# Kernel tuning notes

Hardware: AMD Instinct MI355X
Metric: run time of the kernel (lower is better)

## Reference

```python
import jax, jax.numpy as jnp
import numpy as np

H, S, B, R, IN, NN, OP = 512, 256, 32, 16, 4, 16, 6
NEG = -1.0e12


def setup_inputs() -> dict:
    key = jax.random.key(0)
    ks = jax.random.split(key, 40)
    f32 = jnp.float32
    inp = {}
    inp["node_emb"] = jax.random.normal(ks[0], (B, 1, H), f32)
    inp["left"] = jax.random.normal(ks[1], (B, 1, H), f32)
    inp["encoder_outputs"] = jax.random.normal(ks[2], (S, B, H), f32)
    inp["num_pades"] = jax.random.normal(ks[3], (B, NN, H), f32)
    inp["formula_scores"] = jax.random.normal(ks[4], (R, H), f32)
    inp["has_left"] = jax.random.bernoulli(ks[5], 0.5, (B,))
    lengths = jax.random.randint(ks[6], (B,), S // 2, S + 1)
    inp["seq_mask"] = jnp.arange(S)[None, :] >= lengths[:, None]
    nlen = jax.random.randint(ks[7], (B,), (IN + NN) // 2, IN + NN + 1)
    inp["mask_nums"] = jnp.arange(IN + NN)[None, :] >= nlen[:, None]
    sc = 0.04  # init scale for weights
    def w(i, shape):
        return jax.random.normal(ks[i], shape, f32) * sc
    inp["embedding_weight"] = jax.random.normal(ks[8], (1, IN, H), f32)
    inp["Wcl"] = w(9, (H, H));    inp["bcl"] = jnp.zeros((H,), f32)
    inp["Wclg"] = w(10, (H, H));  inp["bclg"] = jnp.zeros((H,), f32)
    inp["Wcr"] = w(11, (2 * H, H));  inp["bcr"] = jnp.zeros((H,), f32)
    inp["Wcrg"] = w(12, (2 * H, H)); inp["bcrg"] = jnp.zeros((H,), f32)
    inp["Wops"] = w(13, (2 * H, OP)); inp["bops"] = jnp.zeros((OP,), f32)
    inp["Wattn"] = w(14, (2 * H, H)); inp["battn"] = jnp.zeros((H,), f32)
    inp["wattn_s"] = w(15, (H,));     inp["battn_s"] = jnp.zeros((), f32)
    inp["Wfattn"] = w(16, (2 * H, H)); inp["bfattn"] = jnp.zeros((H,), f32)
    inp["wfattn_s"] = w(17, (H,));     inp["bfattn_s"] = jnp.zeros((), f32)
    inp["Wscore"] = w(18, (3 * H, H)); inp["bscore"] = jnp.zeros((H,), f32)
    inp["wscore_s"] = w(19, (H,))  # Score.score has no bias
    inp["Wfp1"] = w(20, (H, H));   inp["bfp1"] = jnp.zeros((H,), f32)
    inp["Wfp2"] = w(21, (H,));     inp["bfp2"] = jnp.zeros((), f32)
    return inp


def _forward(node_emb, left, has_left, encoder_outputs, num_pades, seq_mask,
             mask_nums, formula_scores, embedding_weight, Wcl, bcl, Wclg, bclg,
             Wcr, bcr, Wcrg, bcrg, Wops, bops, Wattn, battn, wattn_s, battn_s,
             Wfattn, bfattn, wfattn_s, bfattn_s, Wscore, bscore, wscore_s,
             Wfp1, bfp1, Wfp2, bfp2):
    # gated left/right node update (dropout = identity, eval mode)
    c = node_emb                                            # [B,1,H]
    lc = jnp.concatenate([left, c], axis=-1)                # [B,1,2H]
    out_l = jnp.tanh(c @ Wcl + bcl) * jax.nn.sigmoid(c @ Wclg + bclg)
    out_r = jnp.tanh(lc @ Wcr + bcr) * jax.nn.sigmoid(lc @ Wcrg + bcrg)
    current_node = jnp.where(has_left[:, None, None], out_r, out_l)  # [B,1,H]
    # TreeAttn(current_node, encoder_outputs): additive attention over S
    Wh, We = Wattn[:H], Wattn[H:]
    feat = jnp.tanh(current_node[:, 0][None] @ Wh + encoder_outputs @ We + battn)  # [S,B,H]
    en = (feat @ wattn_s + battn_s).T                       # [B,S]
    en = jnp.where(seq_mask, NEG, en)
    current_attn = jax.nn.softmax(en, axis=1)[:, None, :]   # [B,1,S]
    eo_b = jnp.transpose(encoder_outputs, (1, 0, 2))        # [B,S,H]
    current_context = current_attn @ eo_b                   # [B,1,H]
    # embedding table = learned constants + numbers from the problem
    emb_w = jnp.concatenate(
        [jnp.broadcast_to(embedding_weight, (node_emb.shape[0], IN, H)), num_pades], axis=1)  # [B,IN+NN,H]
    leaf_input = jnp.concatenate([current_node, current_context], axis=2)[:, 0]  # [B,2H]
    # FormulaAttn: additive attention of each formula over all tokens
    Wfe, Wff = Wfattn[:H], Wfattn[H:]
    ffeat = jnp.tanh(encoder_outputs[None] @ Wfe
                     + (formula_scores @ Wff)[:, None, None, :] + bfattn)  # [R,S,B,H]
    fen = jnp.transpose(ffeat @ wfattn_s + bfattn_s, (2, 0, 1))            # [B,R,S]
    fen = jnp.where(seq_mask[:, None, :], NEG, fen)
    formulas_attn = jax.nn.softmax(fen, axis=-1)            # [B,R,S]
    formulas_context = (formulas_attn + 0.2 * current_attn) @ eo_b         # [B,R,H]
    formula_feat = jnp.tanh(formulas_context @ Wfp1 + bfp1)
    formula_prob = jax.nn.softmax(formula_feat @ Wfp2 + bfp2, axis=-1)     # [B,R]
    # Score over candidate number embeddings
    N = IN + NN
    hid = jnp.broadcast_to(leaf_input[:, None, :], (leaf_input.shape[0], N, 2 * H))
    ein = jnp.concatenate([hid, emb_w], axis=-1)            # [B,N,3H]
    ns = jnp.tanh(ein @ Wscore + bscore) @ wscore_s         # [B,N]
    num_score = jnp.where(mask_nums, NEG, ns)
    op = leaf_input @ Wops + bops                           # [B,OP]
    return (num_score, op, current_node, current_context, emb_w, formula_prob)


def reference(node_emb, left, has_left, encoder_outputs, num_pades, seq_mask,
              mask_nums, formula_scores, embedding_weight, Wcl, bcl, Wclg, bclg,
              Wcr, bcr, Wcrg, bcrg, Wops, bops, Wattn, battn, wattn_s, battn_s,
              Wfattn, bfattn, wfattn_s, bfattn_s, Wscore, bscore, wscore_s,
              Wfp1, bfp1, Wfp2, bfp2):
    return _forward(node_emb, left, has_left, encoder_outputs, num_pades,
                    seq_mask, mask_nums, formula_scores, embedding_weight,
                    Wcl, bcl, Wclg, bclg, Wcr, bcr, Wcrg, bcrg, Wops, bops,
                    Wattn, battn, wattn_s, battn_s, Wfattn, bfattn, wfattn_s,
                    bfattn_s, Wscore, bscore, wscore_s, Wfp1, bfp1, Wfp2, bfp2)
```

## Files before the change

### kernel.cpp

```cpp
#include <hip/hip_runtime.h>
#include <hip/hip_bf16.h>
#include <stdint.h>

#define H 512
#define S 256
#define B 32
#define R 16
#define NEG -1000000000000.0f

typedef unsigned short u16;
typedef short short8 __attribute__((ext_vector_type(8)));
typedef float f32x4 __attribute__((ext_vector_type(4)));

__device__ __forceinline__ float bf2f(u16 u) {
  unsigned int v = ((unsigned int)u) << 16;
  float f; __builtin_memcpy(&f, &v, 4); return f;
}
__device__ __forceinline__ u16 f2u(float x) {
  __hip_bfloat16 h = __float2bfloat16(x);
  u16 u; __builtin_memcpy(&u, &h, 2); return u;
}
__device__ __forceinline__ float ftanh(float x) {
  float e = __expf(2.f * x);
  return 1.f - 2.f * __builtin_amdgcn_rcpf(e + 1.f);
}
__device__ __forceinline__ float ptanh(float x) {
  float xc = fminf(4.f, fmaxf(-4.f, x));
  float x2 = xc * xc;
  float num = xc * (945.f + x2 * (105.f + x2));
  float den = 945.f + x2 * (420.f + 15.f * x2);
  return num * __builtin_amdgcn_rcpf(den);
}
__device__ __forceinline__ float fsig(float x) {
  return __builtin_amdgcn_rcpf(1.f + __expf(-x));
}
__device__ __forceinline__ void gload16(const void* g, void* l) {
  __builtin_amdgcn_global_load_lds(
      (const __attribute__((address_space(1))) unsigned int*)g,
      (__attribute__((address_space(3))) unsigned int*)l, 16, 0, 0);
}

__device__ __forceinline__ void trans_tile(const float* __restrict__ src, int nb, int k0,
                                           u16* __restrict__ dst, int n0, int Krows,
                                           float (*tile)[65], int t) {
  #pragma unroll
  for (int it = 0; it < 16; ++it) {
    int f = it * 256 + t; int r = f >> 6, c = f & 63;
    tile[r][c] = src[(size_t)(k0 + r) * 512 + nb + c];
  }
  __syncthreads();
  #pragma unroll
  for (int it = 0; it < 16; ++it) {
    int f = it * 256 + t; int r = f >> 6, c = f & 63;
    dst[(size_t)(n0 + r) * Krows + k0 + c] = f2u(tile[c][r]);
  }
}

__global__ __launch_bounds__(256) void k_prep1(
    const float* __restrict__ enc, u16* __restrict__ encb, u16* __restrict__ encc,
    const float* __restrict__ Wattn, const float* __restrict__ Wfattn, u16* __restrict__ Wt,
    const float* __restrict__ Wscore, u16* __restrict__ Wt2a, u16* __restrict__ Wt2b,
    const float* __restrict__ Wfp1, u16* __restrict__ Wt3,
    u16* __restrict__ Wt4,
    const float* __restrict__ node_emb, const float* __restrict__ left,
    const int* __restrict__ has_left,
    const float* __restrict__ Wcl, const float* __restrict__ Wclg,
    const float* __restrict__ Wcr, const float* __restrict__ Wcrg,
    float* __restrict__ gp1, float* __restrict__ gp2,
    const float* __restrict__ emb_w, const float* __restrict__ num_pades,
    float* __restrict__ out_embw, u16* __restrict__ embb, u16* __restrict__ leafb) {
  __shared__ float tile[64][65];
  __shared__ float x[128];
  int id = blockIdx.x, t = threadIdx.x;
  if (id < 2048) {
    int i = (id * 256 + t) * 8;
    float4 a = *(const float4*)(enc + i);
    float4 b4 = *(const float4*)(enc + i + 4);
    short8 o;
    o[0] = (short)f2u(a.x); o[1] = (short)f2u(a.y); o[2] = (short)f2u(a.z); o[3] = (short)f2u(a.w);
    o[4] = (short)f2u(b4.x); o[5] = (short)f2u(b4.y); o[6] = (short)f2u(b4.z); o[7] = (short)f2u(b4.w);
    *(short8*)(encb + i) = o;
    int s = i >> 14, b = (i >> 9) & 31, h = i & 511;
    *(short8*)(encc + (((size_t)b << 8) + s) * 512 + h) = o;
  } else if (id < 2176) {
    int f = id - 2048; int gx = f & 15, gy = f >> 4;
    int n0 = gx * 64, k0 = gy * 64;
    const float* src = (n0 < 512) ? (Wattn + 512 * 512) : Wfattn;
    int nb = (n0 < 512) ? n0 : n0 - 512;
    trans_tile(src, nb, k0, Wt, n0, 512, tile, t);
  } else if (id < 2240) {
    int f = id - 2176; int gx = f & 7, gy = f >> 3;
    trans_tile(Wscore + 1024 * 512, gx * 64, gy * 64, Wt2a, gx * 64, 512, tile, t);
  } else if (id < 2368) {
    int f = id - 2240; int gx = f & 7, gy = f >> 3;
    trans_tile(Wscore, gx * 64, gy * 64, Wt2b, gx * 64, 1024, tile, t);
  } else if (id < 2432) {
    int f = id - 2368; int gx = f & 7, gy = f >> 3;
    trans_tile(Wfp1, gx * 64, gy * 64, Wt3, gx * 64, 512, tile, t);
  } else if (id < 2560) {
    int f = id - 2432; int gx = f & 15, gy = f >> 4;
    int n0 = gx * 64, k0 = gy * 64;
    const float* src = (n0 < 512) ? Wattn : (Wfattn + 512 * 512);
    int nb = (n0 < 512) ? n0 : n0 - 512;
    trans_tile(src, nb, k0, Wt4, n0, 512, tile, t);
  } else if (id < 2816) {
    int f = id - 2560;
    int b = f >> 3, kc = f & 7;
    int hl = has_left[b];
    int k0 = kc * 128;
    float* o1 = gp1 + ((size_t)b * 8 + kc) * 512;
    float* o2 = gp2 + ((size_t)b * 8 + kc) * 512;
    if (!hl && kc >= 4) { o1[t] = 0.f; o1[t + 256] = 0.f; o2[t] = 0.f; o2[t + 256] = 0.f; return; }
    if (t < 128) {
      int k = k0 + t;
      x[t] = hl ? (k < 512 ? left[b * 512 + k] : node_emb[b * 512 + k - 512])
                : node_emb[b * 512 + k];
    }
    __syncthreads();
    const float* W1 = hl ? Wcr : Wcl;
    const float* W2 = hl ? Wcrg : Wclg;
    float a1 = 0.f, a2 = 0.f, a3 = 0.f, a4 = 0.f;
    for (int kk = 0; kk < 128; ++kk) {
      float xv = x[kk];
      const float* w1r = W1 + (size_t)(k0 + kk) * 512;
      const float* w2r = W2 + (size_t)(k0 + kk) * 512;
      a1 += xv * w1r[t]; a2 += xv * w1r[t + 256];
      a3 += xv * w2r[t]; a4 += xv * w2r[t + 256];
    }
    o1[t] = a1; o1[t + 256] = a2; o2[t] = a3; o2[t + 256] = a4;
  } else if (id < 3136) {
    int f = id - 2816;
    #pragma unroll
    for (int rr = 0; rr < 2; ++rr) {
      int row = f * 2 + rr;
      int n = row % 20, b = row / 20;
      #pragma unroll
      for (int i = 0; i < 2; ++i) {
        int h = t + 256 * i;
        float v = (n < 4) ? emb_w[n * 512 + h] : num_pades[((size_t)b * 16 + n - 4) * 512 + h];
        out_embw[(size_t)row * 512 + h] = v;
        embb[(size_t)row * 512 + h] = f2u(v);
      }
    }
  } else {
    int f = id - 3136;
    int base = 32 * 1024 + (f * 256 + t) * 16;
    short8 z8 = {0,0,0,0,0,0,0,0};
    *(short8*)(leafb + base) = z8;
    *(short8*)(leafb + base + 8) = z8;
  }
}

template <int FM, int FN>
__device__ __forceinline__ void gemm_body(
    const u16* __restrict__ A, const u16* __restrict__ Bt,
    u16* __restrict__ C16, float* __restrict__ C32,
    int lda, int ldb, int ldc, int ksteps,
    int bm, int bn, int kbase, long zoff,
    u16* As, u16* Bs) {
  constexpr int BM = FM * 32, BN = FN * 32;
  const int tid = threadIdx.x;
  const int lane = tid & 63;
  const int wid = tid >> 6;
  const int wr = (wid >> 1) * (FM * 16);
  const int wc = (wid & 1) * (FN * 16);
  f32x4 acc[FM][FN];
  #pragma unroll
  for (int m = 0; m < FM; ++m)
    #pragma unroll
    for (int n = 0; n < FN; ++n)
      #pragma unroll
      for (int q = 0; q < 4; ++q) acc[m][n][q] = 0.f;

  const int kb = (lane >> 4) * 8;
  const int rr = lane & 15;
  for (int ks = 0; ks < ksteps; ++ks) {
    int k0 = kbase + ks * 32;
    #pragma unroll
    for (int it = 0; it < BM / 64; ++it) {
      int c = it * 256 + tid;
      gload16(A + (size_t)(bm + (c >> 2)) * lda + k0 + (c & 3) * 8, As + c * 8);
    }
    #pragma unroll
    for (int it = 0; it < BN / 64; ++it) {
      int c = it * 256 + tid;
      gload16(Bt + (size_t)(bn + (c >> 2)) * ldb + k0 + (c & 3) * 8, Bs + c * 8);
    }
    __syncthreads();
    short8 af[FM], bf[FN];
    #pragma unroll
    for (int m = 0; m < FM; ++m)
      af[m] = *(const short8*)(As + (wr + m * 16 + rr) * 32 + kb);
    #pragma unroll
    for (int n = 0; n < FN; ++n)
      bf[n] = *(const short8*)(Bs + (wc + n * 16 + rr) * 32 + kb);
    #pragma unroll
    for (int m = 0; m < FM; ++m)
      #pragma unroll
      for (int n = 0; n < FN; ++n)
        acc[m][n] = __builtin_amdgcn_mfma_f32_16x16x32_bf16(af[m], bf[n], acc[m][n], 0, 0, 0);
    __syncthreads();
  }
  int r0 = (lane >> 4) * 4, cc = lane & 15;
  #pragma unroll
  for (int m = 0; m < FM; ++m)
    #pragma unroll
    for (int n = 0; n < FN; ++n)
      #pragma unroll
      for (int q = 0; q < 4; ++q) {
        long row = bm + wr + m * 16 + r0 + q;
        long col = bn + wc + n * 16 + cc;
        if (C16) C16[zoff + row * ldc + col] = f2u(acc[m][n][q]);
        else     C32[zoff + row * ldc + col] = acc[m][n][q];
      }
}

__global__ __launch_bounds__(256) void k_g1(
    const u16* __restrict__ encb, const u16* __restrict__ Wt, u16* __restrict__ EW,
    const u16* __restrict__ cnfs, const u16* __restrict__ Wt4, float* __restrict__ CWFW,
    const u16* __restrict__ embb, const u16* __restrict__ Wt2a, float* __restrict__ Tep) {
  __shared__ u16 As[128 * 32];
  __shared__ u16 Bs[128 * 32];
  int q = blockIdx.x;
  if (q < 512) {
    int x = q & 63, y = q >> 6;
    gemm_body<4, 4>(encb, Wt, EW, nullptr, 512, 512, 1024, 16, x * 128, y * 128, 0, 0, As, Bs);
  } else if (q < 520) {
    int y = q - 512;
    gemm_body<4, 4>(cnfs, Wt4, nullptr, CWFW, 512, 512, 1024, 16, 0, y * 128, 0, 0, As, Bs);
  } else {
    int q2 = q - 520;
    int x = q2 % 10, y = (q2 / 10) % 8, z = q2 / 80;
    gemm_body<2, 2>(embb, Wt2a, nullptr, Tep, 512, 512, 512, 8,
                    x * 64, y * 64, z * 8 * 32, (long)z * 327680, As, Bs);
  }
}

__global__ __launch_bounds__(256) void k_tt(
    const u16* __restrict__ leafb, const u16* __restrict__ Wt2b, float* __restrict__ Tlp,
    const u16* __restrict__ fctxb, const u16* __restrict__ Wt3, float* __restrict__ T3p,
    const float* __restrict__ leaf, const float* __restrict__ Wops,
    const float* __restrict__ bops, float* __restrict__ out_op) {
  __shared__ u16 As[64 * 32];
  __shared__ u16 Bs[64 * 32];
  __shared__ float red[4];
  int q = blockIdx.x;
  if (q < 32) {
    int y = q % 8, z = q / 8;
    gemm_body<2, 2>(leafb, Wt2b, nullptr, Tlp, 1024, 1024, 512, 8,
                    0, y * 64, z * 8 * 32, (long)z * 32768, As, Bs);
  } else if (q < 288) {
    int q2 = q - 32;
    int x = q2 % 8, y = (q2 / 8) % 8, z = q2 / 64;
    gemm_body<2, 2>(fctxb, Wt3, nullptr, T3p, 512, 512, 512, 4,
                    x * 64, y * 64, z * 4 * 32, (long)z * 262144, As, Bs);
  } else {
    int f = q - 288; int o = f % 6, b = f / 6;
    int t = threadIdx.x, w = t >> 6, lane = t & 63;
    float acc = 0.f;
    #pragma unroll
    for (int i = 0; i < 4; ++i) {
      int k = t + 256 * i;
      acc += leaf[b * 1024 + k] * Wops[(size_t)k * 6 + o];
    }
    for (int off = 32; off >= 1; off >>= 1) acc += __shfl_down(acc, off);
    if (lane == 0) red[w] = acc;
    __syncthreads();
    if (t == 0) out_op[b * 6 + o] = red[0] + red[1] + red[2] + red[3] + bops[o];
  }
}

__global__ __launch_bounds__(256) void k_p2(
    const float* __restrict__ gp1, const float* __restrict__ gp2,
    const int* __restrict__ has_left,
    const float* __restrict__ bcl, const float* __restrict__ bclg,
    const float* __restrict__ bcr, const float* __restrict__ bcrg,
    const float* __restrict__ fs,
    float* __restrict__ cur_node, float* __restrict__ out_cn, u16* __restrict__ cnfs) {
  int id = blockIdx.x, t = threadIdx.x;
  if (id < 32) {
    int b = id, hl = has_left[b];
    #pragma unroll
    for (int i = 0; i < 2; ++i) {
      int h = t + 256 * i;
      float s1 = 0.f, s2 = 0.f;
      #pragma unroll
      for (int c = 0; c < 8; ++c) {
        s1 += gp1[((size_t)b * 8 + c) * 512 + h];
        s2 += gp2[((size_t)b * 8 + c) * 512 + h];
      }
      float v = ftanh(s1 + (hl ? bcr[h] : bcl[h])) * fsig(s2 + (hl ? bcrg[h] : bclg[h]));
      cur_node[b * 512 + h] = v;
      out_cn[b * 512 + h] = v;
      cnfs[b * 512 + h] = f2u(v);
    }
  } else if (id < 48) {
    int r = id - 32;
    #pragma unroll
    for (int i = 0; i < 2; ++i) {
      int h = t + 256 * i;
      cnfs[id * 512 + h] = f2u(fs[r * 512 + h]);
    }
  } else {
    #pragma unroll
    for (int i = 0; i < 2; ++i) cnfs[id * 512 + t + 256 * i] = 0;
  }
}

__global__ __launch_bounds__(256) void k_enfen(
    const u16* __restrict__ EW, const float* __restrict__ CWFW,
    const float* __restrict__ battn, const float* __restrict__ bfattn,
    const float* __restrict__ wattn_s, const float* __restrict__ battn_s,
    const float* __restrict__ wfattn_s, const float* __restrict__ bfattn_s,
    const int* __restrict__ seq_mask, float* __restrict__ en, float* __restrict__ fen) {
  __shared__ float sFW[16 * 512];
  __shared__ float swf[512], swa[512], scw[512];
  int bid = blockIdx.x;
  int b = bid >> 5;
  int s0 = (bid & 31) * 8;
  int t = threadIdx.x;
  #pragma unroll
  for (int q = 0; q < 32; ++q) {
    int flat = q * 256 + t;
    int r = flat >> 9, h = flat & 511;
    sFW[flat] = CWFW[(size_t)(32 + r) * 1024 + 512 + h] + bfattn[h];
  }
  swf[t] = wfattn_s[t]; swf[256 + t] = wfattn_s[256 + t];
  swa[t] = wattn_s[t];  swa[256 + t] = wattn_s[256 + t];
  scw[t] = CWFW[(size_t)b * 1024 + t] + battn[t];
  scw[256 + t] = CWFW[(size_t)b * 1024 + 256 + t] + battn[256 + t];
  __syncthreads();
  int w = t >> 6, lane = t & 63;
  int sA = s0 + w * 2, sB = sA + 1;
  int mA = seq_mask[b * 256 + sA], mB = seq_mask[b * 256 + sB];
  if (mA && mB) {
    if (lane == 0) {
      en[b * 256 + sA] = NEG; en[b * 256 + sB] = NEG;
      for (int r = 0; r < 16; ++r) {
        fen[((size_t)b * 16 + r) * 256 + sA] = NEG;
        fen[((size_t)b * 16 + r) * 256 + sB] = NEG;
      }
    }
    return;
  }
  const u16* ewA = EW + (size_t)(sA * 32 + b) * 1024;
  const u16* ewB = EW + (size_t)(sB * 32 + b) * 1024;
  float ewfA[8], ewfB[8], wfv[8];
  float accA = 0.f, accB = 0.f;
  #pragma unroll
  for (int i = 0; i < 8; ++i) {
    int h = lane + 64 * i;
    float cw = scw[h], wa = swa[h];
    accA += ptanh(cw + bf2f(ewA[h])) * wa;
    accB += ptanh(cw + bf2f(ewB[h])) * wa;
    ewfA[i] = bf2f(ewA[512 + h]);
    ewfB[i] = bf2f(ewB[512 + h]);
    wfv[i] = swf[h];
  }
  for (int o = 32; o >= 1; o >>= 1) {
    accA += __shfl_down(accA, o);
    accB += __shfl_down(accB, o);
  }
  if (lane == 0) {
    en[b * 256 + sA] = mA ? NEG : (accA + battn_s[0]);
    en[b * 256 + sB] = mB ? NEG : (accB + battn_s[0]);
  }
  for (int r = 0; r < 16; ++r) {
    float a0 = 0.f, a1 = 0.f;
    #pragma unroll
    for (int i = 0; i < 8; ++i) {
      int h = lane + 64 * i;
      float fwv = sFW[r * 512 + h];
      a0 += ptanh(fwv + ewfA[i]) * wfv[i];
      a1 += ptanh(fwv + ewfB[i]) * wfv[i];
    }
    for (int o = 32; o >= 1; o >>= 1) {
      a0 += __shfl_down(a0, o);
      a1 += __shfl_down(a1, o);
    }
    if (lane == 0) {
      fen[((size_t)b * 16 + r) * 256 + sA] = mA ? NEG : (a0 + bfattn_s[0]);
      fen[((size_t)b * 16 + r) * 256 + sB] = mB ? NEG : (a1 + bfattn_s[0]);
    }
  }
}

__global__ __launch_bounds__(512) void k_ctxall(
    const float* __restrict__ en, const float* __restrict__ fen,
    const u16* __restrict__ encc, const float* __restrict__ cur_node,
    float* __restrict__ out_ctx, float* __restrict__ leaf, u16* __restrict__ fctxb,
    u16* __restrict__ leafb) {
  int br = blockIdx.x;
  int b = br / 9, k = br % 9;
  int t = threadIdx.x;
  __shared__ float red[512];
  __shared__ float sa0[256], sa1[256];
  float xe = (t < 256) ? en[b * 256 + t] : NEG;
  red[t] = xe; __syncthreads();
  for (int o = 256; o > 0; o >>= 1) { if (t < o) red[t] = fmaxf(red[t], red[t + o]); __syncthreads(); }
  float m = red[0]; __syncthreads();
  float ee = (t < 256) ? __expf(xe - m) : 0.f;
  red[t] = ee; __syncthreads();
  for (int o = 256; o > 0; o >>= 1) { if (t < o) red[t] += red[t + o]; __syncthreads(); }
  float attn_v = ee / red[0];
  __syncthreads();
  const u16* eb = encc + (size_t)b * 131072;
  if (k < 8) {
    #pragma unroll
    for (int p = 0; p < 2; ++p) {
      int j = k + p * 8;
      float xf = (t < 256) ? fen[((size_t)b * 16 + j) * 256 + t] : NEG;
      red[t] = xf; __syncthreads();
      for (int o = 256; o > 0; o >>= 1) { if (t < o) red[t] = fmaxf(red[t], red[t + o]); __syncthreads(); }
      float mf = red[0]; __syncthreads();
      float ef = (t < 256) ? __expf(xf - mf) : 0.f;
      red[t] = ef; __syncthreads();
      for (int o = 256; o > 0; o >>= 1) { if (t < o) red[t] += red[t + o]; __syncthreads(); }
      float coef = ef / red[0] + 0.2f * attn_v;
      __syncthreads();
      if (t < 256) { if (p == 0) sa0[t] = coef; else sa1[t] = coef; }
    }
    __syncthreads();
    int h = t;
    float acc0 = 0.f, acc1 = 0.f;
    #pragma unroll 8
    for (int s = 0; s < 256; ++s) {
      float ev = bf2f(eb[(size_t)s * 512 + h]);
      acc0 += sa0[s] * ev;
      acc1 += sa1[s] * ev;
    }
    fctxb[((size_t)b * 16 + k) * 512 + h] = f2u(acc0);
    fctxb[((size_t)b * 16 + k + 8) * 512 + h] = f2u(acc1);
  } else {
    if (t < 256) sa0[t] = attn_v;
    __syncthreads();
    int h = t;
    float acc = 0.f;
    #pragma unroll 8
    for (int s = 0; s < 256; ++s)
      acc += sa0[s] * bf2f(eb[(size_t)s * 512 + h]);
    float cn = cur_node[b * 512 + h];
    out_ctx[b * 512 + h] = acc;
    leaf[b * 1024 + 512 + h] = acc;
    leaf[b * 1024 + h] = cn;
    leafb[b * 1024 + h] = f2u(cn);
    leafb[b * 1024 + 512 + h] = f2u(acc);
  }
}

__global__ __launch_bounds__(256) void k_epi(
    const float* __restrict__ Tep, const float* __restrict__ Tlp,
    const float* __restrict__ bscore,
    const float* __restrict__ wscore_s, const int* __restrict__ mask_nums,
    float* __restrict__ out_ns,
    const float* __restrict__ T3p, const float* __restrict__ bfp1,
    const float* __restrict__ Wfp2, const float* __restrict__ bfp2,
    float* __restrict__ out_fp) {
  int id = blockIdx.x, t = threadIdx.x;
  int w = t >> 6, lane = t & 63;
  __shared__ float red[16];
  if (id < 640) {
    int row = id;
    int b = row / 20;
    float acc = 0.f;
    #pragma unroll
    for (int i = 0; i < 2; ++i) {
      int h = t + 256 * i;
      float tv = bscore[h];
      #pragma unroll
      for (int z = 0; z < 2; ++z) tv += Tep[(size_t)z * 327680 + (size_t)row * 512 + h];
      #pragma unroll
      for (int z = 0; z < 4; ++z) tv += Tlp[(size_t)z * 32768 + (size_t)b * 512 + h];
      acc += ftanh(tv) * wscore_s[h];
    }
    for (int o = 32; o >= 1; o >>= 1) acc += __shfl_down(acc, o);
    if (lane == 0) red[w] = acc;
    __syncthreads();
    if (t == 0) out_ns[row] = mask_nums[row] ? NEG : (red[0] + red[1] + red[2] + red[3]);
  } else {
    int b = id - 640;
    #pragma unroll
    for (int j2 = 0; j2 < 4; ++j2) {
      int j = w * 4 + j2;
      int row = b * 16 + j;
      float acc = 0.f;
      #pragma unroll
      for (int i = 0; i < 8; ++i) {
        int h = lane + 64 * i;
        float v = bfp1[h];
        #pragma unroll
        for (int z = 0; z < 4; ++z) v += T3p[(size_t)z * 262144 + (size_t)row * 512 + h];
        acc += ftanh(v) * Wfp2[h];
      }
      for (int o = 32; o >= 1; o >>= 1) acc += __shfl_down(acc, o);
      if (lane == 0) red[j] = acc + bfp2[0];
    }
    __syncthreads();
    if (t < 16) {
      float xx = red[t];
      float mm = xx;
      for (int o = 8; o >= 1; o >>= 1) mm = fmaxf(mm, __shfl_xor(mm, o, 16));
      float e = __expf(xx - mm);
      float s2 = e;
      for (int o = 8; o >= 1; o >>= 1) s2 += __shfl_xor(s2, o, 16);
      out_fp[b * 16 + t] = e / s2;
    }
  }
}

extern "C" void kernel_launch(void* const* d_in, const int* in_sizes, int n_in,
                              void* d_out, int out_size, void* d_ws, size_t ws_size,
                              hipStream_t stream) {
  const float* node_emb  = (const float*)d_in[0];
  const float* left      = (const float*)d_in[1];
  const float* enc       = (const float*)d_in[2];
  const float* num_pades = (const float*)d_in[3];
  const float* fs        = (const float*)d_in[4];
  const int*   has_left  = (const int*)d_in[5];
  const int*   seq_mask  = (const int*)d_in[6];
  const int*   mask_nums = (const int*)d_in[7];
  const float* emb_w     = (const float*)d_in[8];
  const float* Wcl  = (const float*)d_in[9];
  const float* bcl  = (const float*)d_in[10];
  const float* Wclg = (const float*)d_in[11];
  const float* bclg = (const float*)d_in[12];
  const float* Wcr  = (const float*)d_in[13];
  const float* bcr  = (const float*)d_in[14];
  const float* Wcrg = (const float*)d_in[15];
  const float* bcrg = (const float*)d_in[16];
  const float* Wops = (const float*)d_in[17];
  const float* bops = (const float*)d_in[18];
  const float* Wattn   = (const float*)d_in[19];
  const float* battn   = (const float*)d_in[20];
  const float* wattn_s = (const float*)d_in[21];
  const float* battn_s = (const float*)d_in[22];
  const float* Wfattn   = (const float*)d_in[23];
  const float* bfattn   = (const float*)d_in[24];
  const float* wfattn_s = (const float*)d_in[25];
  const float* bfattn_s = (const float*)d_in[26];
  const float* Wscore   = (const float*)d_in[27];
  const float* bscore   = (const float*)d_in[28];
  const float* wscore_s = (const float*)d_in[29];
  const float* Wfp1 = (const float*)d_in[30];
  const float* bfp1 = (const float*)d_in[31];
  const float* Wfp2 = (const float*)d_in[32];
  const float* bfp2 = (const float*)d_in[33];

  float* out = (float*)d_out;
  float* out_ns   = out + 0;
  float* out_op   = out + 640;
  float* out_cn   = out + 832;
  float* out_ctx  = out + 17216;
  float* out_embw = out + 33600;
  float* out_fp   = out + 361280;

  uint8_t* wsb = (uint8_t*)d_ws;
  u16*   encb = (u16*)(wsb + 0);
  u16*   Wt   = (u16*)(wsb + 8388608);
  u16*   Wt2a = (u16*)(wsb + 9437184);
  u16*   Wt2b = (u16*)(wsb + 9961472);
  u16*   Wt3  = (u16*)(wsb + 11010048);
  u16*   Wt4  = (u16*)(wsb + 11534336);
  u16*   EW   = (u16*)(wsb + 12582912);
  u16*   embb = (u16*)(wsb + 29360128);
  u16*   leafb= (u16*)(wsb + 30015488);
  u16*   cnfs = (u16*)(wsb + 30146560);
  float* CWFW = (float*)(wsb + 30277632);
  float* Tep  = (float*)(wsb + 30801920);
  float* Tlp  = (float*)(wsb + 36044800);
  float* T3p  = (float*)(wsb + 36569088);
  float* fb   = (float*)(wsb + 40763392);
  float* cur_node = fb + 0;
  float* en   = fb + 16384;
  float* fen  = fb + 24576;
  float* leaf = fb + 155648;
  u16*   fctxb= (u16*)(fb + 188416);
  float* gp1  = fb + 319488;
  float* gp2  = fb + 450560;
  u16*   encc = (u16*)(wsb + 45088768);

  k_prep1<<<3144, 256, 0, stream>>>(enc, encb, encc, Wattn, Wfattn, Wt, Wscore, Wt2a, Wt2b,
                                    Wfp1, Wt3, Wt4,
                                    node_emb, left, has_left, Wcl, Wclg, Wcr, Wcrg,
                                    gp1, gp2, emb_w, num_pades, out_embw, embb, leafb);
  k_p2<<<128, 256, 0, stream>>>(gp1, gp2, has_left, bcl, bclg, bcr, bcrg, fs,
                                cur_node, out_cn, cnfs);
  k_g1<<<680, 256, 0, stream>>>(encb, Wt, EW, cnfs, Wt4, CWFW, embb, Wt2a, Tep);
  k_enfen<<<1024, 256, 0, stream>>>(EW, CWFW, battn, bfattn, wattn_s, battn_s,
                                    wfattn_s, bfattn_s, seq_mask, en, fen);
  k_ctxall<<<288, 512, 0, stream>>>(en, fen, encc, cur_node, out_ctx, leaf, fctxb, leafb);
  k_tt<<<480, 256, 0, stream>>>(leafb, Wt2b, Tlp, fctxb, Wt3, T3p,
                                leaf, Wops, bops, out_op);
  k_epi<<<672, 256, 0, stream>>>(Tep, Tlp, bscore, wscore_s, mask_nums, out_ns,
                                 T3p, bfp1, Wfp2, bfp2, out_fp);
}
```

Measured before the change: 99.27 us.

## Coarsen enfen, ctxall and tt kernels to amortize shared setup per block

k_enfen now handles four sequence positions per wavefront instead of two, which halves the blocks that reload the 32KB sFW table from CWFW. k_ctxall computes four formula contexts per block instead of two, so each encoder column read is reused across more accumulators and the repeated softmax over en runs in fewer blocks. The k_tt GEMMs use larger split-K chunks, which halves the partial buffers that k_epi has to sum. In exchange there are fewer blocks, so parallelism and occupancy drop, and the wider kernels use more registers.

```diff
diff --git a/kernel.cpp b/kernel.cpp
--- a/kernel.cpp
+++ b/kernel.cpp
@@ -245,17 +245,17 @@
   __shared__ u16 Bs[64 * 32];
   __shared__ float red[4];
   int q = blockIdx.x;
-  if (q < 32) {
+  if (q < 16) {
     int y = q % 8, z = q / 8;
-    gemm_body<2, 2>(leafb, Wt2b, nullptr, Tlp, 1024, 1024, 512, 8,
-                    0, y * 64, z * 8 * 32, (long)z * 32768, As, Bs);
-  } else if (q < 288) {
-    int q2 = q - 32;
+    gemm_body<2, 2>(leafb, Wt2b, nullptr, Tlp, 1024, 1024, 512, 16,
+                    0, y * 64, z * 16 * 32, (long)z * 32768, As, Bs);
+  } else if (q < 144) {
+    int q2 = q - 16;
     int x = q2 % 8, y = (q2 / 8) % 8, z = q2 / 64;
-    gemm_body<2, 2>(fctxb, Wt3, nullptr, T3p, 512, 512, 512, 4,
-                    x * 64, y * 64, z * 4 * 32, (long)z * 262144, As, Bs);
+    gemm_body<2, 2>(fctxb, Wt3, nullptr, T3p, 512, 512, 512, 8,
+                    x * 64, y * 64, z * 8 * 32, (long)z * 262144, As, Bs);
   } else {
-    int f = q - 288; int o = f % 6, b = f / 6;
+    int f = q - 144; int o = f % 6, b = f / 6;
     int t = threadIdx.x, w = t >> 6, lane = t & 63;
     float acc = 0.f;
     #pragma unroll
@@ -316,8 +316,8 @@
   __shared__ float sFW[16 * 512];
   __shared__ float swf[512], swa[512], scw[512];
   int bid = blockIdx.x;
-  int b = bid >> 5;
-  int s0 = (bid & 31) * 8;
+  int b = bid >> 4;
+  int s0 = (bid & 15) * 16;
   int t = threadIdx.x;
   #pragma unroll
   for (int q = 0; q < 32; ++q) {
@@ -331,56 +331,65 @@
   scw[256 + t] = CWFW[(size_t)b * 1024 + 256 + t] + battn[256 + t];
   __syncthreads();
   int w = t >> 6, lane = t & 63;
-  int sA = s0 + w * 2, sB = sA + 1;
-  int mA = seq_mask[b * 256 + sA], mB = seq_mask[b * 256 + sB];
-  if (mA && mB) {
+  int sbase = s0 + w * 4;
+  int msk[4];
+  int allm = 1;
+  #pragma unroll
+  for (int p = 0; p < 4; ++p) { msk[p] = seq_mask[b * 256 + sbase + p]; allm &= msk[p]; }
+  if (allm) {
     if (lane == 0) {
-      en[b * 256 + sA] = NEG; en[b * 256 + sB] = NEG;
-      for (int r = 0; r < 16; ++r) {
-        fen[((size_t)b * 16 + r) * 256 + sA] = NEG;
-        fen[((size_t)b * 16 + r) * 256 + sB] = NEG;
-      }
+      #pragma unroll
+      for (int p = 0; p < 4; ++p) en[b * 256 + sbase + p] = NEG;
+      for (int r = 0; r < 16; ++r)
+        #pragma unroll
+        for (int p = 0; p < 4; ++p)
+          fen[((size_t)b * 16 + r) * 256 + sbase + p] = NEG;
     }
     return;
   }
-  const u16* ewA = EW + (size_t)(sA * 32 + b) * 1024;
-  const u16* ewB = EW + (size_t)(sB * 32 + b) * 1024;
-  float ewfA[8], ewfB[8], wfv[8];
-  float accA = 0.f, accB = 0.f;
+  const u16* ew[4];
+  #pragma unroll
+  for (int p = 0; p < 4; ++p) ew[p] = EW + (size_t)((sbase + p) * 32 + b) * 1024;
+  float ewf[4][8], wfv[8];
+  float accE[4] = {0.f, 0.f, 0.f, 0.f};
   #pragma unroll
   for (int i = 0; i < 8; ++i) {
     int h = lane + 64 * i;
     float cw = scw[h], wa = swa[h];
-    accA += ptanh(cw + bf2f(ewA[h])) * wa;
-    accB += ptanh(cw + bf2f(ewB[h])) * wa;
-    ewfA[i] = bf2f(ewA[512 + h]);
-    ewfB[i] = bf2f(ewB[512 + h]);
+    #pragma unroll
+    for (int p = 0; p < 4; ++p) {
+      accE[p] += ptanh(cw + bf2f(ew[p][h])) * wa;
+      ewf[p][i] = bf2f(ew[p][512 + h]);
+    }
     wfv[i] = swf[h];
   }
   for (int o = 32; o >= 1; o >>= 1) {
-    accA += __shfl_down(accA, o);
-    accB += __shfl_down(accB, o);
+    #pragma unroll
+    for (int p = 0; p < 4; ++p) accE[p] += __shfl_down(accE[p], o);
   }
   if (lane == 0) {
-    en[b * 256 + sA] = mA ? NEG : (accA + battn_s[0]);
-    en[b * 256 + sB] = mB ? NEG : (accB + battn_s[0]);
+    #pragma unroll
+    for (int p = 0; p < 4; ++p)
+      en[b * 256 + sbase + p] = msk[p] ? NEG : (accE[p] + battn_s[0]);
   }
   for (int r = 0; r < 16; ++r) {
-    float a0 = 0.f, a1 = 0.f;
+    float a[4] = {0.f, 0.f, 0.f, 0.f};
     #pragma unroll
     for (int i = 0; i < 8; ++i) {
       int h = lane + 64 * i;
       float fwv = sFW[r * 512 + h];
-      a0 += ptanh(fwv + ewfA[i]) * wfv[i];
-      a1 += ptanh(fwv + ewfB[i]) * wfv[i];
+      float wf = wfv[i];
+      #pragma unroll
+      for (int p = 0; p < 4; ++p) a[p] += ptanh(fwv + ewf[p][i]) * wf;
     }
     for (int o = 32; o >= 1; o >>= 1) {
-      a0 += __shfl_down(a0, o);
-      a1 += __shfl_down(a1, o);
+      #pragma unroll
+      for (int p = 0; p < 4; ++p) a[p] += __shfl_down(a[p], o);
     }
     if (lane == 0) {
-      fen[((size_t)b * 16 + r) * 256 + sA] = mA ? NEG : (a0 + bfattn_s[0]);
-      fen[((size_t)b * 16 + r) * 256 + sB] = mB ? NEG : (a1 + bfattn_s[0]);
+      #pragma unroll
+      for (int p = 0; p < 4; ++p)
+        fen[((size_t)b * 16 + r) * 256 + sbase + p] = msk[p] ? NEG : (a[p] + bfattn_s[0]);
     }
   }
 }
@@ -391,10 +400,10 @@
     float* __restrict__ out_ctx, float* __restrict__ leaf, u16* __restrict__ fctxb,
     u16* __restrict__ leafb) {
   int br = blockIdx.x;
-  int b = br / 9, k = br % 9;
+  int b = br / 5, k = br % 5;
   int t = threadIdx.x;
   __shared__ float red[512];
-  __shared__ float sa0[256], sa1[256];
+  __shared__ float sa[4][256];
   float xe = (t < 256) ? en[b * 256 + t] : NEG;
   red[t] = xe; __syncthreads();
   for (int o = 256; o > 0; o >>= 1) { if (t < o) red[t] = fmaxf(red[t], red[t + o]); __syncthreads(); }
@@ -405,10 +414,10 @@
   float attn_v = ee / red[0];
   __syncthreads();
   const u16* eb = encc + (size_t)b * 131072;
-  if (k < 8) {
-    #pragma unroll
-    for (int p = 0; p < 2; ++p) {
-      int j = k + p * 8;
+  if (k < 4) {
+    #pragma unroll
+    for (int p = 0; p < 4; ++p) {
+      int j = k + p * 4;
       float xf = (t < 256) ? fen[((size_t)b * 16 + j) * 256 + t] : NEG;
       red[t] = xf; __syncthreads();
       for (int o = 256; o > 0; o >>= 1) { if (t < o) red[t] = fmaxf(red[t], red[t + o]); __syncthreads(); }
@@ -418,27 +427,31 @@
       for (int o = 256; o > 0; o >>= 1) { if (t < o) red[t] += red[t + o]; __syncthreads(); }
       float coef = ef / red[0] + 0.2f * attn_v;
       __syncthreads();
-      if (t < 256) { if (p == 0) sa0[t] = coef; else sa1[t] = coef; }
+      if (t < 256) sa[p][t] = coef;
     }
     __syncthreads();
     int h = t;
-    float acc0 = 0.f, acc1 = 0.f;
-    #pragma unroll 8
+    float acc0 = 0.f, acc1 = 0.f, acc2 = 0.f, acc3 = 0.f;
+    #pragma unroll 4
     for (int s = 0; s < 256; ++s) {
       float ev = bf2f(eb[(size_t)s * 512 + h]);
-      acc0 += sa0[s] * ev;
-      acc1 += sa1[s] * ev;
+      acc0 += sa[0][s] * ev;
+      acc1 += sa[1][s] * ev;
+      acc2 += sa[2][s] * ev;
+      acc3 += sa[3][s] * ev;
     }
     fctxb[((size_t)b * 16 + k) * 512 + h] = f2u(acc0);
-    fctxb[((size_t)b * 16 + k + 8) * 512 + h] = f2u(acc1);
+    fctxb[((size_t)b * 16 + k + 4) * 512 + h] = f2u(acc1);
+    fctxb[((size_t)b * 16 + k + 8) * 512 + h] = f2u(acc2);
+    fctxb[((size_t)b * 16 + k + 12) * 512 + h] = f2u(acc3);
   } else {
-    if (t < 256) sa0[t] = attn_v;
+    if (t < 256) sa[0][t] = attn_v;
     __syncthreads();
     int h = t;
     float acc = 0.f;
     #pragma unroll 8
     for (int s = 0; s < 256; ++s)
-      acc += sa0[s] * bf2f(eb[(size_t)s * 512 + h]);
+      acc += sa[0][s] * bf2f(eb[(size_t)s * 512 + h]);
     float cn = cur_node[b * 512 + h];
     out_ctx[b * 512 + h] = acc;
     leaf[b * 1024 + 512 + h] = acc;
@@ -470,7 +483,7 @@
       #pragma unroll
       for (int z = 0; z < 2; ++z) tv += Tep[(size_t)z * 327680 + (size_t)row * 512 + h];
       #pragma unroll
-      for (int z = 0; z < 4; ++z) tv += Tlp[(size_t)z * 32768 + (size_t)b * 512 + h];
+      for (int z = 0; z < 2; ++z) tv += Tlp[(size_t)z * 32768 + (size_t)b * 512 + h];
       acc += ftanh(tv) * wscore_s[h];
     }
     for (int o = 32; o >= 1; o >>= 1) acc += __shfl_down(acc, o);
@@ -489,7 +502,7 @@
         int h = lane + 64 * i;
         float v = bfp1[h];
         #pragma unroll
-        for (int z = 0; z < 4; ++z) v += T3p[(size_t)z * 262144 + (size_t)row * 512 + h];
+        for (int z = 0; z < 2; ++z) v += T3p[(size_t)z * 262144 + (size_t)row * 512 + h];
         acc += ftanh(v) * Wfp2[h];
       }
       for (int o = 32; o >= 1; o >>= 1) acc += __shfl_down(acc, o);
@@ -586,10 +599,10 @@
   k_p2<<<128, 256, 0, stream>>>(gp1, gp2, has_left, bcl, bclg, bcr, bcrg, fs,
                                 cur_node, out_cn, cnfs);
   k_g1<<<680, 256, 0, stream>>>(encb, Wt, EW, cnfs, Wt4, CWFW, embb, Wt2a, Tep);
-  k_enfen<<<1024, 256, 0, stream>>>(EW, CWFW, battn, bfattn, wattn_s, battn_s,
-                                    wfattn_s, bfattn_s, seq_mask, en, fen);
-  k_ctxall<<<288, 512, 0, stream>>>(en, fen, encc, cur_node, out_ctx, leaf, fctxb, leafb);
-  k_tt<<<480, 256, 0, stream>>>(leafb, Wt2b, Tlp, fctxb, Wt3, T3p,
+  k_enfen<<<512, 256, 0, stream>>>(EW, CWFW, battn, bfattn, wattn_s, battn_s,
+                                   wfattn_s, bfattn_s, seq_mask, en, fen);
+  k_ctxall<<<160, 512, 0, stream>>>(en, fen, encc, cur_node, out_ctx, leaf, fctxb, leafb);
+  k_tt<<<336, 256, 0, stream>>>(leafb, Wt2b, Tlp, fctxb, Wt3, T3p,
                                 leaf, Wops, bops, out_op);
   k_epi<<<672, 256, 0, stream>>>(Tep, Tlp, bscore, wscore_s, mask_nums, out_ns,
                                  T3p, bfp1, Wfp2, bfp2, out_fp);
```

Result: slower. 116.3 us (+17.1%).
